# Kernel tuning notes

Hardware: AMD Instinct MI355X
Metric: run time of the kernel (lower is better)

Reference implementation:

```python
import jax, jax.numpy as jnp
import numpy as np


def setup_inputs() -> dict:
    key = jax.random.key(0)
    k0, k1, k2, k3 = jax.random.split(key, 4)
    B, S, D, F, E = 2, 2048, 1024, 4096, 8
    hidden_states = jax.random.normal(k0, (B, S, D), dtype=jnp.float32)
    Wr = jax.random.normal(k1, (E, D), dtype=jnp.float32) * 0.02   # router Linear weight [E, D]
    W1 = jax.random.normal(k2, (E, D, F), dtype=jnp.float32) * 0.02  # expert w1 (transposed torch layout)
    W2 = jax.random.normal(k3, (E, F, D), dtype=jnp.float32) * 0.02  # expert w2
    return {"hidden_states": hidden_states, "Wr": Wr, "W1": W1, "W2": W2, "top_k": 2}


def reference(hidden_states, Wr, W1, W2, top_k):
    # hidden_states: [B, S, D]; Wr: [E, D]; W1: [E, D, F]; W2: [E, F, D]
    E = Wr.shape[0]
    dt = hidden_states.dtype

    # Router: logits -> top-k expert indices. NOTE: the original module computes
    # softmax routing weights over the top-k logits but never applies them in the
    # combine step, so the output is an UNWEIGHTED sum over selected experts.
    router_logits = jnp.einsum('bsd,ed->bse', hidden_states, Wr)
    _, topk_idx = jax.lax.top_k(router_logits, top_k)            # [B, S, K]

    # mask[b,s,e] = 1 if expert e is in token (b,s)'s top-k (indices are distinct)
    mask = (jax.nn.one_hot(topk_idx, E, dtype=dt).sum(axis=-2) > 0).astype(dt)  # [B, S, E]

    # Dense per-expert FFN (SiLU MLP, no bias, dropout=identity in eval):
    h = jax.nn.silu(jnp.einsum('bsd,edf->bsef', hidden_states, W1))  # [B, S, E, F]
    y = jnp.einsum('bsef,efd->bsed', h, W2)                          # [B, S, E, D]

    # Combine: unweighted sum over selected experts (faithful to source)
    return jnp.einsum('bsed,bse->bsd', y, mask)
```

## Files before the change

kernel.cpp:

```cpp
#include <hip/hip_runtime.h>
#include <hip/hip_bf16.h>
#include <stdint.h>

#define TOKENS 4096
#define DDIM 1024
#define FDIM 4096
#define NEXP 8
#define BM 128
#define BN 128
#define BK 64

typedef __attribute__((ext_vector_type(4))) float f32x4;
typedef __attribute__((ext_vector_type(8))) short short8;

__device__ __forceinline__ unsigned short f2bf(float f) {
    union { float f; uint32_t u; } v; v.f = f;
    uint32_t u = v.u;
    return (unsigned short)((u + 0x7fff + ((u >> 16) & 1)) >> 16);
}

#define BARRIER() asm volatile("s_barrier" ::: "memory")
#define WAIT_VM0() asm volatile("s_waitcnt vmcnt(0)" ::: "memory")
#define GLDS(SRC, DST) __builtin_amdgcn_global_load_lds( \
    (const __attribute__((address_space(1))) void*)(SRC), \
    (__attribute__((address_space(3))) void*)(DST), 16, 0, 0)

__global__ __launch_bounds__(256) void cvt_x(const float* __restrict__ x,
                                             unsigned short* __restrict__ xb, int n) {
    int i = (blockIdx.x * 256 + threadIdx.x) * 8;
    if (i >= n) return;
    float4 a = *(const float4*)(x + i);
    float4 b = *(const float4*)(x + i + 4);
    short8 o;
    o[0] = f2bf(a.x); o[1] = f2bf(a.y); o[2] = f2bf(a.z); o[3] = f2bf(a.w);
    o[4] = f2bf(b.x); o[5] = f2bf(b.y); o[6] = f2bf(b.z); o[7] = f2bf(b.w);
    *(short8*)(xb + i) = o;
}

__global__ __launch_bounds__(256) void transpose_cvt(const float* __restrict__ in,
                                                     unsigned short* __restrict__ out,
                                                     int R, int C) {
    __shared__ float tile[32][33];
    int e = blockIdx.z;
    int r0 = blockIdx.y * 32, c0 = blockIdx.x * 32;
    const float* src = in + (size_t)e * R * C;
    unsigned short* dst = out + (size_t)e * R * C;
    int t = threadIdx.x;
    int rr = t >> 3;
    int cc = (t & 7) * 4;
    float4 v = *(const float4*)(src + (size_t)(r0 + rr) * C + c0 + cc);
    tile[rr][cc + 0] = v.x; tile[rr][cc + 1] = v.y;
    tile[rr][cc + 2] = v.z; tile[rr][cc + 3] = v.w;
    __syncthreads();
    int oc = rr;
    int orr = cc;
    ushort4 o;
    o.x = f2bf(tile[orr + 0][oc]);
    o.y = f2bf(tile[orr + 1][oc]);
    o.z = f2bf(tile[orr + 2][oc]);
    o.w = f2bf(tile[orr + 3][oc]);
    *(ushort4*)(dst + (size_t)(c0 + oc) * R + r0 + orr) = o;
}

__global__ __launch_bounds__(256) void router(const float* __restrict__ x,
                                              const float* __restrict__ wr,
                                              int* __restrict__ cnt,
                                              int* __restrict__ list) {
    __shared__ float wl[NEXP * DDIM];
    int t = threadIdx.x;
    for (int i = t; i < NEXP * DDIM; i += 256) wl[i] = wr[i];
    __syncthreads();
    int tok = blockIdx.x * 4 + (t >> 6);
    int lane = t & 63;
    float acc[NEXP];
#pragma unroll
    for (int e = 0; e < NEXP; e++) acc[e] = 0.f;
    const float* xr = x + (size_t)tok * DDIM;
    for (int d = lane; d < DDIM; d += 64) {
        float xv = xr[d];
#pragma unroll
        for (int e = 0; e < NEXP; e++) acc[e] += xv * wl[e * DDIM + d];
    }
#pragma unroll
    for (int e = 0; e < NEXP; e++) {
#pragma unroll
        for (int off = 32; off; off >>= 1) acc[e] += __shfl_xor(acc[e], off);
    }
    if (lane == 0) {
        int e1 = 0; float v1 = acc[0];
        for (int e = 1; e < NEXP; e++) if (acc[e] > v1) { v1 = acc[e]; e1 = e; }
        int e2 = -1; float v2 = -1e30f;
        for (int e = 0; e < NEXP; e++) if (e != e1 && acc[e] > v2) { v2 = acc[e]; e2 = e; }
        int p1 = atomicAdd(&cnt[e1], 1);
        list[e1 * TOKENS + p1] = tok;
        int p2 = atomicAdd(&cnt[e2], 1);
        list[e2 * TOKENS + p2] = tok;
    }
}

__global__ void setup(const int* __restrict__ cnt, int* __restrict__ off,
                      int* __restrict__ wbA, int* __restrict__ wbB,
                      int* __restrict__ qctr, int* __restrict__ tot) {
    if (threadIdx.x == 0) {
        int s = 0, ta = 0, tb = 0;
        for (int e = 0; e < NEXP; e++) {
            off[e] = s; s += cnt[e];
            wbA[e] = ta; wbB[e] = tb;
            int nt = (cnt[e] + BM - 1) / BM;
            ta += nt * (FDIM / BN);
            tb += nt * (DDIM / BN);
        }
        wbA[NEXP] = ta; wbB[NEXP] = tb;
        tot[0] = ta; tot[1] = tb;
        qctr[0] = 0; qctr[1] = 0;
    }
}

template <bool GATHER_A, bool SILU>
__global__ __launch_bounds__(256, 2) void gemm_moe3(
    const unsigned short* __restrict__ Abase,
    const unsigned short* __restrict__ Wt,
    const int* __restrict__ cnt, const int* __restrict__ off,
    const int* __restrict__ list,
    const int* __restrict__ wbase,
    int* __restrict__ qctr, const int* __restrict__ tot,
    unsigned short* __restrict__ Hout,
    float* __restrict__ Yout,
    int KD, int NDIM) {
    __shared__ alignas(16) unsigned short As[2][BM * BK];
    __shared__ alignas(16) unsigned short Bs[2][BN * BK];
    __shared__ int wsh;

    int t = threadIdx.x;
    int lane = t & 63;
    int wid = t >> 6;
    int wm = wid >> 1, wn = wid & 1;
    int r16 = lane & 15, g = lane >> 4;
    const int total = *tot;

#define FRAG(TILE, ROW, KC) (*(const short8*)&(TILE)[(ROW) * BK + ((((KC)) ^ ((ROW) & 7)) << 3)])

    for (;;) {
        if (t == 0) wsh = atomicAdd(qctr, 1);
        __syncthreads();
        int w = wsh;
        if (w >= total) break;

        int e = 0;
        while (e < NEXP - 1 && w >= wbase[e + 1]) e++;
        w -= wbase[e];
        int n_e = cnt[e];
        int ntm = (n_e + BM - 1) >> 7;
        int by = w / ntm;
        int mtile = w - by * ntm;
        int m0 = mtile * BM;
        int n0 = by * BN;
        int base = off[e];

        const unsigned short* pA[4];
        const unsigned short* pB[4];
        int ldsA[4], ldsB[4];
#pragma unroll
        for (int i = 0; i < 4; i++) {
            int c = i * 256 + t;
            int row = c >> 3, cc = c & 7;
            int arow = m0 + row; if (arow >= n_e) arow = n_e - 1;
            size_t grow = GATHER_A ? (size_t)list[e * TOKENS + arow] : (size_t)(base + arow);
            pA[i] = Abase + grow * (size_t)KD + ((cc ^ (row & 7)) << 3);
            ldsA[i] = c * 16;
            pB[i] = Wt + ((size_t)e * NDIM + n0 + row) * (size_t)KD + ((cc ^ (row & 7)) << 3);
            ldsB[i] = c * 16;
        }

        f32x4 acc[4][4];
#pragma unroll
        for (int i = 0; i < 4; i++)
#pragma unroll
            for (int j = 0; j < 4; j++) acc[i][j] = f32x4{0.f, 0.f, 0.f, 0.f};

#pragma unroll
        for (int i = 0; i < 4; i++) { GLDS(pB[i], (char*)Bs[0] + ldsB[i]); pB[i] += BK; }
#pragma unroll
        for (int i = 0; i < 4; i++) { GLDS(pA[i], (char*)As[0] + ldsA[i]); pA[i] += BK; }
        WAIT_VM0();
        BARRIER();

        const int NT = KD / BK;
        for (int tk = 0; tk < NT; ++tk) {
            const unsigned short* Ac = As[tk & 1];
            const unsigned short* Bc = Bs[tk & 1];
            char* Ad = (char*)As[(tk & 1) ^ 1];
            char* Bd = (char*)Bs[(tk & 1) ^ 1];
            const bool pf = (tk + 1 < NT);

            if (pf) {
#pragma unroll
                for (int i = 0; i < 4; i++) { GLDS(pB[i], Bd + ldsB[i]); pB[i] += BK; }
#pragma unroll
                for (int i = 0; i < 4; i++) { GLDS(pA[i], Ad + ldsA[i]); pA[i] += BK; }
            }

            short8 a0, a1, a2, a3, b0, b1, b2, b3;
            a0 = FRAG(Ac, wm * 64 + 0 * 16 + r16, g);
            a1 = FRAG(Ac, wm * 64 + 1 * 16 + r16, g);
            a2 = FRAG(Ac, wm * 64 + 2 * 16 + r16, g);
            a3 = FRAG(Ac, wm * 64 + 3 * 16 + r16, g);
            b0 = FRAG(Bc, wn * 64 + 0 * 16 + r16, g);
            b1 = FRAG(Bc, wn * 64 + 1 * 16 + r16, g);
            b2 = FRAG(Bc, wn * 64 + 2 * 16 + r16, g);
            b3 = FRAG(Bc, wn * 64 + 3 * 16 + r16, g);
            __builtin_amdgcn_s_setprio(1);
            acc[0][0] = __builtin_amdgcn_mfma_f32_16x16x32_bf16(a0, b0, acc[0][0], 0, 0, 0);
            acc[0][1] = __builtin_amdgcn_mfma_f32_16x16x32_bf16(a0, b1, acc[0][1], 0, 0, 0);
            acc[0][2] = __builtin_amdgcn_mfma_f32_16x16x32_bf16(a0, b2, acc[0][2], 0, 0, 0);
            acc[0][3] = __builtin_amdgcn_mfma_f32_16x16x32_bf16(a0, b3, acc[0][3], 0, 0, 0);
            acc[1][0] = __builtin_amdgcn_mfma_f32_16x16x32_bf16(a1, b0, acc[1][0], 0, 0, 0);
            acc[1][1] = __builtin_amdgcn_mfma_f32_16x16x32_bf16(a1, b1, acc[1][1], 0, 0, 0);
            acc[1][2] = __builtin_amdgcn_mfma_f32_16x16x32_bf16(a1, b2, acc[1][2], 0, 0, 0);
            acc[1][3] = __builtin_amdgcn_mfma_f32_16x16x32_bf16(a1, b3, acc[1][3], 0, 0, 0);
            acc[2][0] = __builtin_amdgcn_mfma_f32_16x16x32_bf16(a2, b0, acc[2][0], 0, 0, 0);
            acc[2][1] = __builtin_amdgcn_mfma_f32_16x16x32_bf16(a2, b1, acc[2][1], 0, 0, 0);
            acc[2][2] = __builtin_amdgcn_mfma_f32_16x16x32_bf16(a2, b2, acc[2][2], 0, 0, 0);
            acc[2][3] = __builtin_amdgcn_mfma_f32_16x16x32_bf16(a2, b3, acc[2][3], 0, 0, 0);
            acc[3][0] = __builtin_amdgcn_mfma_f32_16x16x32_bf16(a3, b0, acc[3][0], 0, 0, 0);
            acc[3][1] = __builtin_amdgcn_mfma_f32_16x16x32_bf16(a3, b1, acc[3][1], 0, 0, 0);
            acc[3][2] = __builtin_amdgcn_mfma_f32_16x16x32_bf16(a3, b2, acc[3][2], 0, 0, 0);
            acc[3][3] = __builtin_amdgcn_mfma_f32_16x16x32_bf16(a3, b3, acc[3][3], 0, 0, 0);
            __builtin_amdgcn_s_setprio(0);
            a0 = FRAG(Ac, wm * 64 + 0 * 16 + r16, 4 + g);
            a1 = FRAG(Ac, wm * 64 + 1 * 16 + r16, 4 + g);
            a2 = FRAG(Ac, wm * 64 + 2 * 16 + r16, 4 + g);
            a3 = FRAG(Ac, wm * 64 + 3 * 16 + r16, 4 + g);
            b0 = FRAG(Bc, wn * 64 + 0 * 16 + r16, 4 + g);
            b1 = FRAG(Bc, wn * 64 + 1 * 16 + r16, 4 + g);
            b2 = FRAG(Bc, wn * 64 + 2 * 16 + r16, 4 + g);
            b3 = FRAG(Bc, wn * 64 + 3 * 16 + r16, 4 + g);
            __builtin_amdgcn_s_setprio(1);
            acc[0][0] = __builtin_amdgcn_mfma_f32_16x16x32_bf16(a0, b0, acc[0][0], 0, 0, 0);
            acc[0][1] = __builtin_amdgcn_mfma_f32_16x16x32_bf16(a0, b1, acc[0][1], 0, 0, 0);
            acc[0][2] = __builtin_amdgcn_mfma_f32_16x16x32_bf16(a0, b2, acc[0][2], 0, 0, 0);
            acc[0][3] = __builtin_amdgcn_mfma_f32_16x16x32_bf16(a0, b3, acc[0][3], 0, 0, 0);
            acc[1][0] = __builtin_amdgcn_mfma_f32_16x16x32_bf16(a1, b0, acc[1][0], 0, 0, 0);
            acc[1][1] = __builtin_amdgcn_mfma_f32_16x16x32_bf16(a1, b1, acc[1][1], 0, 0, 0);
            acc[1][2] = __builtin_amdgcn_mfma_f32_16x16x32_bf16(a1, b2, acc[1][2], 0, 0, 0);
            acc[1][3] = __builtin_amdgcn_mfma_f32_16x16x32_bf16(a1, b3, acc[1][3], 0, 0, 0);
            acc[2][0] = __builtin_amdgcn_mfma_f32_16x16x32_bf16(a2, b0, acc[2][0], 0, 0, 0);
            acc[2][1] = __builtin_amdgcn_mfma_f32_16x16x32_bf16(a2, b1, acc[2][1], 0, 0, 0);
            acc[2][2] = __builtin_amdgcn_mfma_f32_16x16x32_bf16(a2, b2, acc[2][2], 0, 0, 0);
            acc[2][3] = __builtin_amdgcn_mfma_f32_16x16x32_bf16(a2, b3, acc[2][3], 0, 0, 0);
            acc[3][0] = __builtin_amdgcn_mfma_f32_16x16x32_bf16(a3, b0, acc[3][0], 0, 0, 0);
            acc[3][1] = __builtin_amdgcn_mfma_f32_16x16x32_bf16(a3, b1, acc[3][1], 0, 0, 0);
            acc[3][2] = __builtin_amdgcn_mfma_f32_16x16x32_bf16(a3, b2, acc[3][2], 0, 0, 0);
            acc[3][3] = __builtin_amdgcn_mfma_f32_16x16x32_bf16(a3, b3, acc[3][3], 0, 0, 0);
            __builtin_amdgcn_s_setprio(0);

            if (pf) WAIT_VM0();
            BARRIER();
        }

#pragma unroll
        for (int mi = 0; mi < 4; ++mi) {
#pragma unroll
            for (int nj = 0; nj < 4; ++nj) {
#pragma unroll
                for (int qq = 0; qq < 4; ++qq) {
                    int lr = wm * 64 + mi * 16 + g * 4 + qq;
                    if (m0 + lr < n_e) {
                        int col = n0 + wn * 64 + nj * 16 + r16;
                        float v = acc[mi][nj][qq];
                        if (SILU) {
                            v = v / (1.f + __expf(-v));
                            Hout[(size_t)(base + m0 + lr) * NDIM + col] = f2bf(v);
                        } else {
                            int tok = list[e * TOKENS + m0 + lr];
                            atomicAdd(&Yout[(size_t)tok * NDIM + col], v);
                        }
                    }
                }
            }
        }
    }
#undef FRAG
}

extern "C" void kernel_launch(void* const* d_in, const int* in_sizes, int n_in,
                              void* d_out, int out_size, void* d_ws, size_t ws_size,
                              hipStream_t stream) {
    const float* X  = (const float*)d_in[0];
    const float* Wr = (const float*)d_in[1];
    const float* W1 = (const float*)d_in[2];
    const float* W2 = (const float*)d_in[3];
    float* Y = (float*)d_out;

    char* ws = (char*)d_ws;
    int* cnt  = (int*)(ws + 0);
    int* off  = (int*)(ws + 64);
    int* wbA  = (int*)(ws + 128);
    int* wbB  = (int*)(ws + 192);
    int* qctr = (int*)(ws + 256);
    int* tot  = (int*)(ws + 288);
    int* list = (int*)(ws + 1024);
    unsigned short* Xb = (unsigned short*)(ws + (1ull << 20));
    unsigned short* WT = (unsigned short*)(ws + (16ull << 20));
    unsigned short* H  = (unsigned short*)(ws + (80ull << 20));

    hipMemsetAsync(d_out, 0, (size_t)out_size * sizeof(float), stream);
    hipMemsetAsync(cnt, 0, 32, stream);

    cvt_x<<<TOKENS * DDIM / (256 * 8), 256, 0, stream>>>(X, Xb, TOKENS * DDIM);
    router<<<TOKENS / 4, 256, 0, stream>>>(X, Wr, cnt, list);
    setup<<<1, 64, 0, stream>>>(cnt, off, wbA, wbB, qctr, tot);

    transpose_cvt<<<dim3(FDIM / 32, DDIM / 32, NEXP), 256, 0, stream>>>(W1, WT, DDIM, FDIM);
    gemm_moe3<true, true><<<512, 256, 0, stream>>>(
        Xb, WT, cnt, off, list, wbA, qctr + 0, tot + 0, H, nullptr, DDIM, FDIM);

    transpose_cvt<<<dim3(DDIM / 32, FDIM / 32, NEXP), 256, 0, stream>>>(W2, WT, FDIM, DDIM);
    gemm_moe3<false, false><<<512, 256, 0, stream>>>(
        H, WT, cnt, off, list, wbB, qctr + 1, tot + 1, nullptr, Y, FDIM, DDIM);
}
```

Measured before the change: 492.1 us.

## Switch expert GEMM to 4-stage BK=32 LDS pipeline with partial vmcnt waits

The grouped MoE GEMM goes from a double-buffered BK=64 LDS scheme to four LDS stages of BK=32, keeping three tile loads in flight. Instead of draining all outstanding loads each iteration, it waits with vmcnt(8), vmcnt(4) or vmcnt(0) so only the stage about to be consumed must be ready. The LDS swizzle is redone for the 64-byte rows. Total LDS use is unchanged, but there are twice as many barriers and half as many MFMAs between them, so sync overhead may cancel the gain from hiding global-load latency.

```diff
diff --git a/kernel.cpp b/kernel.cpp
--- a/kernel.cpp
+++ b/kernel.cpp
@@ -8,7 +8,7 @@
 #define NEXP 8
 #define BM 128
 #define BN 128
-#define BK 64
+#define BK2 32
 
 typedef __attribute__((ext_vector_type(4))) float f32x4;
 typedef __attribute__((ext_vector_type(8))) short short8;
@@ -21,6 +21,8 @@
 
 #define BARRIER() asm volatile("s_barrier" ::: "memory")
 #define WAIT_VM0() asm volatile("s_waitcnt vmcnt(0)" ::: "memory")
+#define WAIT_VM4() asm volatile("s_waitcnt vmcnt(4)" ::: "memory")
+#define WAIT_VM8() asm volatile("s_waitcnt vmcnt(8)" ::: "memory")
 #define GLDS(SRC, DST) __builtin_amdgcn_global_load_lds( \
     (const __attribute__((address_space(1))) void*)(SRC), \
     (__attribute__((address_space(3))) void*)(DST), 16, 0, 0)
@@ -117,7 +119,7 @@
 }
 
 template <bool GATHER_A, bool SILU>
-__global__ __launch_bounds__(256, 2) void gemm_moe3(
+__global__ __launch_bounds__(256, 2) void gemm_moe4(
     const unsigned short* __restrict__ Abase,
     const unsigned short* __restrict__ Wt,
     const int* __restrict__ cnt, const int* __restrict__ off,
@@ -127,8 +129,8 @@
     unsigned short* __restrict__ Hout,
     float* __restrict__ Yout,
     int KD, int NDIM) {
-    __shared__ alignas(16) unsigned short As[2][BM * BK];
-    __shared__ alignas(16) unsigned short Bs[2][BN * BK];
+    __shared__ alignas(16) unsigned short As[4][BM * BK2];
+    __shared__ alignas(16) unsigned short Bs[4][BN * BK2];
     __shared__ int wsh;
 
     int t = threadIdx.x;
@@ -138,7 +140,7 @@
     int r16 = lane & 15, g = lane >> 4;
     const int total = *tot;
 
-#define FRAG(TILE, ROW, KC) (*(const short8*)&(TILE)[(ROW) * BK + ((((KC)) ^ ((ROW) & 7)) << 3)])
+#define FRAG32(TILE, ROW, G) (*(const short8*)&(TILE)[(ROW) * BK2 + ((((G) ^ (((ROW) >> 1) & 3))) << 3)])
 
     for (;;) {
         if (t == 0) wsh = atomicAdd(qctr, 1);
@@ -157,19 +159,19 @@
         int n0 = by * BN;
         int base = off[e];
 
-        const unsigned short* pA[4];
-        const unsigned short* pB[4];
-        int ldsA[4], ldsB[4];
-#pragma unroll
-        for (int i = 0; i < 4; i++) {
+        const unsigned short* pA[2];
+        const unsigned short* pB[2];
+        int ldsOff[2];
+#pragma unroll
+        for (int i = 0; i < 2; i++) {
             int c = i * 256 + t;
-            int row = c >> 3, cc = c & 7;
+            int row = c >> 2, p = c & 3;
+            int cg = p ^ ((row >> 1) & 3);
             int arow = m0 + row; if (arow >= n_e) arow = n_e - 1;
             size_t grow = GATHER_A ? (size_t)list[e * TOKENS + arow] : (size_t)(base + arow);
-            pA[i] = Abase + grow * (size_t)KD + ((cc ^ (row & 7)) << 3);
-            ldsA[i] = c * 16;
-            pB[i] = Wt + ((size_t)e * NDIM + n0 + row) * (size_t)KD + ((cc ^ (row & 7)) << 3);
-            ldsB[i] = c * 16;
+            pA[i] = Abase + grow * (size_t)KD + (cg << 3);
+            pB[i] = Wt + ((size_t)e * NDIM + n0 + row) * (size_t)KD + (cg << 3);
+            ldsOff[i] = c * 16;
         }
 
         f32x4 acc[4][4];
@@ -179,36 +181,38 @@
             for (int j = 0; j < 4; j++) acc[i][j] = f32x4{0.f, 0.f, 0.f, 0.f};
 
 #pragma unroll
-        for (int i = 0; i < 4; i++) { GLDS(pB[i], (char*)Bs[0] + ldsB[i]); pB[i] += BK; }
-#pragma unroll
-        for (int i = 0; i < 4; i++) { GLDS(pA[i], (char*)As[0] + ldsA[i]); pA[i] += BK; }
-        WAIT_VM0();
+        for (int s = 0; s < 3; ++s) {
+#pragma unroll
+            for (int i = 0; i < 2; i++) { GLDS(pA[i], (char*)As[s] + ldsOff[i]); pA[i] += BK2; }
+#pragma unroll
+            for (int i = 0; i < 2; i++) { GLDS(pB[i], (char*)Bs[s] + ldsOff[i]); pB[i] += BK2; }
+        }
+        WAIT_VM8();
         BARRIER();
 
-        const int NT = KD / BK;
+        const int NT = KD / BK2;
         for (int tk = 0; tk < NT; ++tk) {
-            const unsigned short* Ac = As[tk & 1];
-            const unsigned short* Bc = Bs[tk & 1];
-            char* Ad = (char*)As[(tk & 1) ^ 1];
-            char* Bd = (char*)Bs[(tk & 1) ^ 1];
-            const bool pf = (tk + 1 < NT);
-
-            if (pf) {
-#pragma unroll
-                for (int i = 0; i < 4; i++) { GLDS(pB[i], Bd + ldsB[i]); pB[i] += BK; }
-#pragma unroll
-                for (int i = 0; i < 4; i++) { GLDS(pA[i], Ad + ldsA[i]); pA[i] += BK; }
+            const int rs = tk & 3;
+            const unsigned short* Ac = As[rs];
+            const unsigned short* Bc = Bs[rs];
+
+            if (tk + 3 < NT) {
+                const int ws_ = (tk + 3) & 3;
+#pragma unroll
+                for (int i = 0; i < 2; i++) { GLDS(pA[i], (char*)As[ws_] + ldsOff[i]); pA[i] += BK2; }
+#pragma unroll
+                for (int i = 0; i < 2; i++) { GLDS(pB[i], (char*)Bs[ws_] + ldsOff[i]); pB[i] += BK2; }
             }
 
             short8 a0, a1, a2, a3, b0, b1, b2, b3;
-            a0 = FRAG(Ac, wm * 64 + 0 * 16 + r16, g);
-            a1 = FRAG(Ac, wm * 64 + 1 * 16 + r16, g);
-            a2 = FRAG(Ac, wm * 64 + 2 * 16 + r16, g);
-            a3 = FRAG(Ac, wm * 64 + 3 * 16 + r16, g);
-            b0 = FRAG(Bc, wn * 64 + 0 * 16 + r16, g);
-            b1 = FRAG(Bc, wn * 64 + 1 * 16 + r16, g);
-            b2 = FRAG(Bc, wn * 64 + 2 * 16 + r16, g);
-            b3 = FRAG(Bc, wn * 64 + 3 * 16 + r16, g);
+            a0 = FRAG32(Ac, wm * 64 + 0 * 16 + r16, g);
+            a1 = FRAG32(Ac, wm * 64 + 1 * 16 + r16, g);
+            a2 = FRAG32(Ac, wm * 64 + 2 * 16 + r16, g);
+            a3 = FRAG32(Ac, wm * 64 + 3 * 16 + r16, g);
+            b0 = FRAG32(Bc, wn * 64 + 0 * 16 + r16, g);
+            b1 = FRAG32(Bc, wn * 64 + 1 * 16 + r16, g);
+            b2 = FRAG32(Bc, wn * 64 + 2 * 16 + r16, g);
+            b3 = FRAG32(Bc, wn * 64 + 3 * 16 + r16, g);
             __builtin_amdgcn_s_setprio(1);
             acc[0][0] = __builtin_amdgcn_mfma_f32_16x16x32_bf16(a0, b0, acc[0][0], 0, 0, 0);
             acc[0][1] = __builtin_amdgcn_mfma_f32_16x16x32_bf16(a0, b1, acc[0][1], 0, 0, 0);
@@ -227,35 +231,13 @@
             acc[3][2] = __builtin_amdgcn_mfma_f32_16x16x32_bf16(a3, b2, acc[3][2], 0, 0, 0);
             acc[3][3] = __builtin_amdgcn_mfma_f32_16x16x32_bf16(a3, b3, acc[3][3], 0, 0, 0);
             __builtin_amdgcn_s_setprio(0);
-            a0 = FRAG(Ac, wm * 64 + 0 * 16 + r16, 4 + g);
-            a1 = FRAG(Ac, wm * 64 + 1 * 16 + r16, 4 + g);
-            a2 = FRAG(Ac, wm * 64 + 2 * 16 + r16, 4 + g);
-            a3 = FRAG(Ac, wm * 64 + 3 * 16 + r16, 4 + g);
-            b0 = FRAG(Bc, wn * 64 + 0 * 16 + r16, 4 + g);
-            b1 = FRAG(Bc, wn * 64 + 1 * 16 + r16, 4 + g);
-            b2 = FRAG(Bc, wn * 64 + 2 * 16 + r16, 4 + g);
-            b3 = FRAG(Bc, wn * 64 + 3 * 16 + r16, 4 + g);
-            __builtin_amdgcn_s_setprio(1);
-            acc[0][0] = __builtin_amdgcn_mfma_f32_16x16x32_bf16(a0, b0, acc[0][0], 0, 0, 0);
-            acc[0][1] = __builtin_amdgcn_mfma_f32_16x16x32_bf16(a0, b1, acc[0][1], 0, 0, 0);
-            acc[0][2] = __builtin_amdgcn_mfma_f32_16x16x32_bf16(a0, b2, acc[0][2], 0, 0, 0);
-            acc[0][3] = __builtin_amdgcn_mfma_f32_16x16x32_bf16(a0, b3, acc[0][3], 0, 0, 0);
-            acc[1][0] = __builtin_amdgcn_mfma_f32_16x16x32_bf16(a1, b0, acc[1][0], 0, 0, 0);
-            acc[1][1] = __builtin_amdgcn_mfma_f32_16x16x32_bf16(a1, b1, acc[1][1], 0, 0, 0);
-            acc[1][2] = __builtin_amdgcn_mfma_f32_16x16x32_bf16(a1, b2, acc[1][2], 0, 0, 0);
-            acc[1][3] = __builtin_amdgcn_mfma_f32_16x16x32_bf16(a1, b3, acc[1][3], 0, 0, 0);
-            acc[2][0] = __builtin_amdgcn_mfma_f32_16x16x32_bf16(a2, b0, acc[2][0], 0, 0, 0);
-            acc[2][1] = __builtin_amdgcn_mfma_f32_16x16x32_bf16(a2, b1, acc[2][1], 0, 0, 0);
-            acc[2][2] = __builtin_amdgcn_mfma_f32_16x16x32_bf16(a2, b2, acc[2][2], 0, 0, 0);
-            acc[2][3] = __builtin_amdgcn_mfma_f32_16x16x32_bf16(a2, b3, acc[2][3], 0, 0, 0);
-            acc[3][0] = __builtin_amdgcn_mfma_f32_16x16x32_bf16(a3, b0, acc[3][0], 0, 0, 0);
-            acc[3][1] = __builtin_amdgcn_mfma_f32_16x16x32_bf16(a3, b1, acc[3][1], 0, 0, 0);
-            acc[3][2] = __builtin_amdgcn_mfma_f32_16x16x32_bf16(a3, b2, acc[3][2], 0, 0, 0);
-            acc[3][3] = __builtin_amdgcn_mfma_f32_16x16x32_bf16(a3, b3, acc[3][3], 0, 0, 0);
-            __builtin_amdgcn_s_setprio(0);
-
-            if (pf) WAIT_VM0();
-            BARRIER();
+
+            if (tk + 1 < NT) {
+                if (tk + 3 < NT)      WAIT_VM8();
+                else if (tk + 2 < NT) WAIT_VM4();
+                else                  WAIT_VM0();
+                BARRIER();
+            }
         }
 
 #pragma unroll
@@ -280,7 +262,7 @@
             }
         }
     }
-#undef FRAG
+#undef FRAG32
 }
 
 extern "C" void kernel_launch(void* const* d_in, const int* in_sizes, int n_in,
@@ -312,10 +294,10 @@
     setup<<<1, 64, 0, stream>>>(cnt, off, wbA, wbB, qctr, tot);
 
     transpose_cvt<<<dim3(FDIM / 32, DDIM / 32, NEXP), 256, 0, stream>>>(W1, WT, DDIM, FDIM);
-    gemm_moe3<true, true><<<512, 256, 0, stream>>>(
+    gemm_moe4<true, true><<<512, 256, 0, stream>>>(
         Xb, WT, cnt, off, list, wbA, qctr + 0, tot + 0, H, nullptr, DDIM, FDIM);
 
     transpose_cvt<<<dim3(DDIM / 32, FDIM / 32, NEXP), 256, 0, stream>>>(W2, WT, FDIM, DDIM);
-    gemm_moe3<false, false><<<512, 256, 0, stream>>>(
+    gemm_moe4<false, false><<<512, 256, 0, stream>>>(
         H, WT, cnt, off, list, wbB, qctr + 1, tot + 1, nullptr, Y, FDIM, DDIM);
 }
```

After: 555.2 us. 1.13x slower.
